# Performance work log

Measured on AMD Instinct MI355X. Metric: run time of the kernel, lower is better.

The kernel has to match this reference:

```python
import jax, jax.numpy as jnp
import numpy as np

N_VOX = 100000
C_IN = 32
C_OUT = 64
GRID = 96  # voxel grid extent per axis
K = 27     # 3x3x3 kernel offsets
BN_EPS = 1e-5


def _build_neighbor_idx(rng):
    """Sample N_VOX unique active voxels in a GRID^3 volume and build the
    rulebook: for each voxel, the row index of each of its 27 neighbors
    (kernel offsets in {-1,0,1}^3), or -1 if that neighbor is inactive."""
    total = GRID ** 3
    flat = rng.choice(total, size=N_VOX, replace=False).astype(np.int64)
    z = flat // (GRID * GRID)
    y = (flat // GRID) % GRID
    x = flat % GRID
    # dense lookup table: flat coord -> row index (or -1)
    lut = np.full(total, -1, dtype=np.int32)
    lut[flat] = np.arange(N_VOX, dtype=np.int32)
    offs = np.array([(dz, dy, dx)
                     for dz in (-1, 0, 1)
                     for dy in (-1, 0, 1)
                     for dx in (-1, 0, 1)], dtype=np.int64)  # [27,3]
    nz = z[:, None] + offs[None, :, 0]
    ny = y[:, None] + offs[None, :, 1]
    nx = x[:, None] + offs[None, :, 2]
    inb = ((nz >= 0) & (nz < GRID) & (ny >= 0) & (ny < GRID)
           & (nx >= 0) & (nx < GRID))
    nflat = np.where(inb, nz * GRID * GRID + ny * GRID + nx, 0)
    nidx = lut[nflat]                       # [N,27]
    nidx = np.where(inb, nidx, -1).astype(np.int32)
    return nidx


def setup_inputs() -> dict:
    key = jax.random.key(0)
    k_f, k_w = jax.random.split(key)
    rng = np.random.default_rng(0)
    neighbor_idx = jnp.asarray(_build_neighbor_idx(rng))  # [N,27] int32
    features = jax.random.normal(k_f, (N_VOX, C_IN), dtype=jnp.float32)
    # per-kernel-offset conv weights, kaiming-ish scale
    W = jax.random.normal(k_w, (K, C_IN, C_OUT), dtype=jnp.float32)
    W = W * (2.0 / (K * C_IN)) ** 0.5
    gamma = jnp.ones((C_OUT,), dtype=jnp.float32)
    beta = jnp.zeros((C_OUT,), dtype=jnp.float32)
    return {"features": features, "neighbor_idx": neighbor_idx,
            "W": W, "gamma": gamma, "beta": beta}


def reference(features, neighbor_idx, W, gamma, beta):
    # --- sparse (submanifold) 3D conv: gather -> GEMM ---
    mask = neighbor_idx >= 0                               # [N,27]
    safe_idx = jnp.where(mask, neighbor_idx, 0)
    gathered = features[safe_idx]                          # [N,27,Cin]
    gathered = gathered * mask[..., None].astype(features.dtype)
    out = jnp.einsum('nkc,kcd->nd', gathered, W)           # [N,Cout]
    # --- batch norm over active voxels (training-mode stats) ---
    mean = jnp.mean(out, axis=0)
    var = jnp.var(out, axis=0)
    out = (out - mean) * jax.lax.rsqrt(var + BN_EPS) * gamma + beta
    # --- ReLU ---
    return jax.nn.relu(out)
```

## Files before the change

### kernel.cpp

```cpp
#include <hip/hip_runtime.h>
#include <hip/hip_bf16.h>

#define N_VOX 100000
#define C_IN  32
#define C_OUT 64
#define KOFF  27
#define CONV_T 512
#define GRID_C 256
#define VPB    256
#define NT     391
#define NB_FB  782
#define WT_BLOCKS 216
#define WT_HALFS (KOFF * C_OUT * C_IN)
#define WT_BYTES (WT_HALFS * 2)

typedef __attribute__((ext_vector_type(8))) short bf16x8_t;
typedef __attribute__((ext_vector_type(4))) float f32x4_t;

__device__ __forceinline__ short f2bf(float f) {
    __hip_bfloat16 h = __float2bfloat16(f);
    return __builtin_bit_cast(short, h);
}
__device__ __forceinline__ float bf2f(unsigned short u) {
    return __builtin_bit_cast(float, (unsigned)u << 16);
}

__global__ void prep_kernel(const float* __restrict__ W,
                            unsigned short* __restrict__ Wt,
                            const float* __restrict__ feat,
                            unsigned short* __restrict__ fb) {
    int bid = blockIdx.x;
    if (bid < WT_BLOCKS) {
        int i = bid * 256 + threadIdx.x;
        int c = i & 31;
        int d = (i >> 5) & 63;
        int k = i >> 11;
        int dst = i ^ ((d & 7) << 3);
        Wt[dst] = (unsigned short)f2bf(W[k * (C_IN * C_OUT) + c * C_OUT + d]);
    } else {
        int t = (bid - WT_BLOCKS) * 256 + threadIdx.x;
        const int total8 = ((N_VOX + 1) * C_IN) / 8;
        if (t >= total8) return;
        int e = t * 8;
        bf16x8_t o;
        if (e < N_VOX * C_IN) {
            const f32x4_t* fp = (const f32x4_t*)(feat + e);
            f32x4_t f0 = fp[0], f1 = fp[1];
            o[0] = f2bf(f0[0]); o[1] = f2bf(f0[1]); o[2] = f2bf(f0[2]); o[3] = f2bf(f0[3]);
            o[4] = f2bf(f1[0]); o[5] = f2bf(f1[1]); o[6] = f2bf(f1[2]); o[7] = f2bf(f1[3]);
        } else {
            o = (bf16x8_t)(short)0;
        }
        *(bf16x8_t*)(fb + e) = o;
    }
}

#define GLOAD(dst, voff)                                                      \
    asm volatile("global_load_dwordx4 %0, %1, %2"                             \
                 : "=v"(dst) : "v"(voff), "s"(feat_bf))

#define VMW(n) do {                                                           \
    asm volatile("s_waitcnt vmcnt(" #n ")" ::: "memory");                     \
    __builtin_amdgcn_sched_barrier(0);                                        \
} while (0)

template <bool OUTBF>
__global__ __launch_bounds__(CONV_T, 2) void conv_kernel(
    const unsigned short* __restrict__ feat_bf,
    const int* __restrict__ nidx,
    const unsigned short* __restrict__ WtG,
    float* __restrict__ outf, unsigned short* __restrict__ outb,
    float* __restrict__ partials)
{
    __shared__ unsigned short wt_lds[WT_HALFS];
    __shared__ float lsum[8][C_OUT];
    __shared__ float lsq[8][C_OUT];

    const int tid  = threadIdx.x;
    const int wid  = tid >> 6;
    const int lane = tid & 63;
    const int colr = lane & 15;
    const int kch  = lane >> 4;

    for (int j = tid; j < WT_HALFS / 8; j += CONV_T)
        ((bf16x8_t*)wt_lds)[j] = ((const bf16x8_t*)WtG)[j];
    __syncthreads();

    float psum[4] = {0.f, 0.f, 0.f, 0.f};
    float psq[4]  = {0.f, 0.f, 0.f, 0.f};

    const int b  = blockIdx.x;
    const int bs = ((b & 7) << 5) | (b >> 3);
    const int rr0 = NT % GRID_C;
    const int t0  = bs + (bs < rr0 ? bs : rr0);
    const int cnt = 1 + (bs < rr0 ? 1 : 0);

    for (int ti = 0; ti < cnt; ++ti) {
        const int base = (t0 + ti) * VPB + wid * 32;

        unsigned off[54];
        #pragma unroll
        for (int m = 0; m < 2; ++m) {
            int vx = base + m * 16 + colr;
            bool val = vx < N_VOX;
            const int* nr = nidx + (val ? vx : 0) * KOFF;
            int force = val ? 0 : -1;
            #pragma unroll
            for (int k = 0; k < KOFF; ++k) {
                int id = nr[k] | force;
                int s = (id < 0) ? N_VOX : id;
                off[k * 2 + m] = ((unsigned)s << 6) + (unsigned)(kch << 4);
            }
        }
        __builtin_amdgcn_sched_barrier(0);

        f32x4_t acc0[4], acc1[4];
        #pragma unroll
        for (int t = 0; t < 4; ++t) { acc0[t] = (f32x4_t)0.0f; acc1[t] = (f32x4_t)0.0f; }

        bf16x8_t a[12];
        #pragma unroll
        for (int u = 0; u < 12; ++u) GLOAD(a[u], off[u]);
        __builtin_amdgcn_sched_barrier(0);

        #pragma unroll
        for (int c = 0; c < 9; ++c) {
            if (c < 8) { VMW(6); } else { VMW(0); }
            const int ab = (c & 1) * 6;
            #pragma unroll
            for (int j = 0; j < 3; ++j) {
                const int kk = c * 3 + j;
                #pragma unroll
                for (int t = 0; t < 4; ++t) {
                    const int rw = t * 16 + colr;
                    int o = (kk << 12) + (rw << 6) + (kch << 4);
                    o ^= (rw & 7) << 4;
                    bf16x8_t bb = *(const bf16x8_t*)((const char*)wt_lds + o);
                    acc0[t] = __builtin_amdgcn_mfma_f32_16x16x32_bf16(
                        a[ab + j * 2 + 0], bb, acc0[t], 0, 0, 0);
                    acc1[t] = __builtin_amdgcn_mfma_f32_16x16x32_bf16(
                        a[ab + j * 2 + 1], bb, acc1[t], 0, 0, 0);
                }
            }
            if (c + 2 < 9) {
                const int nb2 = ((c + 2) & 1) * 6;
                #pragma unroll
                for (int u = 0; u < 6; ++u) GLOAD(a[nb2 + u], off[(c + 2) * 6 + u]);
                __builtin_amdgcn_sched_barrier(0);
            }
        }

        #pragma unroll
        for (int t = 0; t < 4; ++t) {
            #pragma unroll
            for (int i = 0; i < 4; ++i) {
                int v0 = base + kch * 4 + i;
                int v1 = v0 + 16;
                int ch = t * 16 + colr;
                float x0 = acc0[t][i], x1 = acc1[t][i];
                if (v0 < N_VOX) {
                    if constexpr (OUTBF) outb[v0 * C_OUT + ch] = (unsigned short)f2bf(x0);
                    else                 outf[v0 * C_OUT + ch] = x0;
                }
                if (v1 < N_VOX) {
                    if constexpr (OUTBF) outb[v1 * C_OUT + ch] = (unsigned short)f2bf(x1);
                    else                 outf[v1 * C_OUT + ch] = x1;
                }
                psum[t] += x0 + x1;
                psq[t]  += x0 * x0 + x1 * x1;
            }
        }
    }

    #pragma unroll
    for (int t = 0; t < 4; ++t) {
        psum[t] += __shfl_xor(psum[t], 16);
        psum[t] += __shfl_xor(psum[t], 32);
        psq[t]  += __shfl_xor(psq[t], 16);
        psq[t]  += __shfl_xor(psq[t], 32);
    }
    if (lane < 16) {
        #pragma unroll
        for (int t = 0; t < 4; ++t) {
            lsum[wid][t * 16 + lane] = psum[t];
            lsq[wid][t * 16 + lane]  = psq[t];
        }
    }
    __syncthreads();
    if (tid < 128) {
        int c = tid & 63;
        float s = 0.f;
        if (tid < 64) {
            #pragma unroll
            for (int w = 0; w < 8; ++w) s += lsum[w][c];
        } else {
            #pragma unroll
            for (int w = 0; w < 8; ++w) s += lsq[w][c];
        }
        partials[tid * GRID_C + b] = s;
    }
}

__global__ __launch_bounds__(CONV_T) void conv_fb_kernel(
    const float* __restrict__ feat,
    const int* __restrict__ nidx,
    const unsigned short* __restrict__ WtG,
    float* __restrict__ outf, float* __restrict__ partials)
{
    __shared__ unsigned short wt_lds[WT_HALFS];
    __shared__ float lsum[8][C_OUT];
    __shared__ float lsq[8][C_OUT];

    const int tid  = threadIdx.x;
    const int wid  = tid >> 6;
    const int lane = tid & 63;
    const int colr = lane & 15;
    const int kch  = lane >> 4;
    const int base = blockIdx.x * 128 + wid * 16;
    const int vox  = base + colr;
    const bool valid = (vox < N_VOX);
    const int* nrow = nidx + (valid ? vox : 0) * KOFF;

    for (int j = tid; j < WT_HALFS / 8; j += CONV_T)
        ((bf16x8_t*)wt_lds)[j] = ((const bf16x8_t*)WtG)[j];
    __syncthreads();

    f32x4_t acc[4];
    #pragma unroll
    for (int t = 0; t < 4; ++t) acc[t] = (f32x4_t)0.0f;

    for (int k = 0; k < KOFF; ++k) {
        int idx = valid ? nrow[k] : -1;
        bf16x8_t av = (bf16x8_t)(short)0;
        if (idx >= 0) {
            const f32x4_t* fp = (const f32x4_t*)(feat + (idx << 5) + kch * 8);
            f32x4_t f0 = fp[0], f1 = fp[1];
            av[0] = f2bf(f0[0]); av[1] = f2bf(f0[1]);
            av[2] = f2bf(f0[2]); av[3] = f2bf(f0[3]);
            av[4] = f2bf(f1[0]); av[5] = f2bf(f1[1]);
            av[6] = f2bf(f1[2]); av[7] = f2bf(f1[3]);
        }
        #pragma unroll
        for (int t = 0; t < 4; ++t) {
            int rw = t * 16 + colr;
            int o = (k << 12) + (rw << 6) + (kch << 4);
            o ^= (rw & 7) << 4;
            bf16x8_t bb = *(const bf16x8_t*)((const char*)wt_lds + o);
            acc[t] = __builtin_amdgcn_mfma_f32_16x16x32_bf16(av, bb, acc[t], 0, 0, 0);
        }
    }

    float psum[4], psq[4];
    #pragma unroll
    for (int t = 0; t < 4; ++t) { psum[t] = 0.f; psq[t] = 0.f; }
    #pragma unroll
    for (int t = 0; t < 4; ++t) {
        #pragma unroll
        for (int i = 0; i < 4; ++i) {
            int v = base + kch * 4 + i;
            float x = acc[t][i];
            if (v < N_VOX) outf[v * C_OUT + t * 16 + colr] = x;
            psum[t] += x;
            psq[t]  += x * x;
        }
    }
    #pragma unroll
    for (int t = 0; t < 4; ++t) {
        psum[t] += __shfl_xor(psum[t], 16);
        psum[t] += __shfl_xor(psum[t], 32);
        psq[t]  += __shfl_xor(psq[t], 16);
        psq[t]  += __shfl_xor(psq[t], 32);
    }
    if (lane < 16) {
        #pragma unroll
        for (int t = 0; t < 4; ++t) {
            lsum[wid][t * 16 + lane] = psum[t];
            lsq[wid][t * 16 + lane]  = psq[t];
        }
    }
    __syncthreads();
    if (tid < 128) {
        int c = tid & 63;
        float s = 0.f;
        if (tid < 64) {
            #pragma unroll
            for (int w = 0; w < 8; ++w) s += lsum[w][c];
        } else {
            #pragma unroll
            for (int w = 0; w < 8; ++w) s += lsq[w][c];
        }
        partials[tid * NB_FB + blockIdx.x] = s;
    }
}

__global__ __launch_bounds__(256) void stats_kernel(
    const float* __restrict__ partials, int nb,
    const float* __restrict__ gamma, const float* __restrict__ beta,
    float* __restrict__ ss)
{
    __shared__ float bs[4], bq[4];
    const int c = blockIdx.x;
    const float* ps = partials + c * nb;
    const float* pq = partials + (64 + c) * nb;
    float s = 0.f, q = 0.f;
    for (int i = threadIdx.x; i < nb; i += 256) {
        s += ps[i];
        q += pq[i];
    }
    #pragma unroll
    for (int o = 1; o < 64; o <<= 1) {
        s += __shfl_xor(s, o);
        q += __shfl_xor(q, o);
    }
    int wid = threadIdx.x >> 6, lane = threadIdx.x & 63;
    if (lane == 0) { bs[wid] = s; bq[wid] = q; }
    __syncthreads();
    if (threadIdx.x == 0) {
        float S = bs[0] + bs[1] + bs[2] + bs[3];
        float Q = bq[0] + bq[1] + bq[2] + bq[3];
        float mean = S * (1.0f / N_VOX);
        float var  = Q * (1.0f / N_VOX) - mean * mean;
        float inv  = rsqrtf(var + 1e-5f);
        float sc   = gamma[c] * inv;
        ss[c]      = sc;
        ss[64 + c] = beta[c] - mean * sc;
    }
}

__global__ void bn_relu_b_kernel(const unsigned short* __restrict__ cbf,
                                 const float* __restrict__ ss,
                                 float* __restrict__ out) {
    int i = blockIdx.x * 256 + threadIdx.x;
    bf16x8_t v = ((const bf16x8_t*)cbf)[i];
    int d0 = (i * 8) & 63;
    f32x4_t sc0 = *(const f32x4_t*)(ss + d0);
    f32x4_t sc1 = *(const f32x4_t*)(ss + d0 + 4);
    f32x4_t sh0 = *(const f32x4_t*)(ss + 64 + d0);
    f32x4_t sh1 = *(const f32x4_t*)(ss + 64 + d0 + 4);
    f32x4_t o0, o1;
    #pragma unroll
    for (int j = 0; j < 4; ++j) {
        o0[j] = fmaxf(bf2f((unsigned short)v[j]) * sc0[j] + sh0[j], 0.f);
        o1[j] = fmaxf(bf2f((unsigned short)v[j + 4]) * sc1[j] + sh1[j], 0.f);
    }
    ((f32x4_t*)out)[2 * i]     = o0;
    ((f32x4_t*)out)[2 * i + 1] = o1;
}

__global__ void bn_relu_f_kernel(float* __restrict__ out,
                                 const float* __restrict__ ss) {
    int i = blockIdx.x * 256 + threadIdx.x;
    f32x4_t v = ((f32x4_t*)out)[i];
    int d0 = (i * 4) & 63;
    f32x4_t sc = *(const f32x4_t*)(ss + d0);
    f32x4_t sh = *(const f32x4_t*)(ss + 64 + d0);
    #pragma unroll
    for (int j = 0; j < 4; ++j) v[j] = fmaxf(v[j] * sc[j] + sh[j], 0.f);
    ((f32x4_t*)out)[i] = v;
}

extern "C" void kernel_launch(void* const* d_in, const int* in_sizes, int n_in,
                              void* d_out, int out_size, void* d_ws, size_t ws_size,
                              hipStream_t stream) {
    const float* feat  = (const float*)d_in[0];
    const int*   nidx  = (const int*)d_in[1];
    const float* W     = (const float*)d_in[2];
    const float* gamma = (const float*)d_in[3];
    const float* beta  = (const float*)d_in[4];
    float* out = (float*)d_out;

    char* ws = (char*)d_ws;
    const size_t wt_bytes  = WT_BYTES;
    const size_t fb_bytes  = (size_t)(N_VOX + 1) * C_IN * 2;
    const size_t cb_bytes  = (size_t)N_VOX * C_OUT * 2;
    const size_t pt_bytes  = (size_t)128 * NB_FB * 4;

    const bool bf_ok  = ws_size >= wt_bytes + fb_bytes + pt_bytes + 512;
    const bool cb_ok  = ws_size >= wt_bytes + fb_bytes + cb_bytes + pt_bytes + 512;

    unsigned short* Wt = (unsigned short*)ws;
    unsigned short* feat_bf = (unsigned short*)(ws + wt_bytes);
    unsigned short* cbf = (unsigned short*)(ws + wt_bytes + fb_bytes);
    float* partials;
    if (cb_ok)       partials = (float*)(ws + wt_bytes + fb_bytes + cb_bytes);
    else if (bf_ok)  partials = (float*)(ws + wt_bytes + fb_bytes);
    else             partials = (float*)(ws + wt_bytes);
    float* ss = partials + 128 * NB_FB;

    if (bf_ok) {
        int feat_blocks = (((N_VOX + 1) * C_IN) / 8 + 255) / 256;
        prep_kernel<<<WT_BLOCKS + feat_blocks, 256, 0, stream>>>(W, Wt, feat, feat_bf);
        if (cb_ok)
            conv_kernel<true><<<GRID_C, CONV_T, 0, stream>>>(
                feat_bf, nidx, Wt, out, cbf, partials);
        else
            conv_kernel<false><<<GRID_C, CONV_T, 0, stream>>>(
                feat_bf, nidx, Wt, out, cbf, partials);
        stats_kernel<<<C_OUT, 256, 0, stream>>>(partials, GRID_C, gamma, beta, ss);
    } else {
        prep_kernel<<<WT_BLOCKS, 256, 0, stream>>>(W, Wt, feat, Wt);
        conv_fb_kernel<<<NB_FB, CONV_T, 0, stream>>>(feat, nidx, Wt, out, partials);
        stats_kernel<<<C_OUT, 256, 0, stream>>>(partials, NB_FB, gamma, beta, ss);
    }
    if (cb_ok)
        bn_relu_b_kernel<<<N_VOX * C_OUT / 8 / 256, 256, 0, stream>>>(cbf, ss, out);
    else
        bn_relu_f_kernel<<<N_VOX * C_OUT / 4 / 256, 256, 0, stream>>>(out, ss);
}
```

Measured before the change: 42.48 us.

## Fuse conv, BN statistics and BN+ReLU via grid-wide atomic barrier

```diff
diff --git a/kernel.cpp b/kernel.cpp
--- a/kernel.cpp
+++ b/kernel.cpp
@@ -20,9 +20,6 @@
 __device__ __forceinline__ short f2bf(float f) {
     __hip_bfloat16 h = __float2bfloat16(f);
     return __builtin_bit_cast(short, h);
-}
-__device__ __forceinline__ float bf2f(unsigned short u) {
-    return __builtin_bit_cast(float, (unsigned)u << 16);
 }
 
 __global__ void prep_kernel(const float* __restrict__ W,
@@ -64,13 +61,84 @@
     __builtin_amdgcn_sched_barrier(0);                                        \
 } while (0)
 
-template <bool OUTBF>
-__global__ __launch_bounds__(CONV_T, 2) void conv_kernel(
+__device__ __forceinline__ void process_tile(
+    int tileIdx, const unsigned short* __restrict__ feat_bf,
+    const int* __restrict__ nidx, const unsigned short* wt_lds,
+    int wid, int colr, int kch,
+    f32x4_t (&acc0)[4], f32x4_t (&acc1)[4],
+    float (&psum)[4], float (&psq)[4])
+{
+    const int base = tileIdx * VPB + wid * 32;
+
+    unsigned off[54];
+    #pragma unroll
+    for (int m = 0; m < 2; ++m) {
+        int vx = base + m * 16 + colr;
+        bool val = vx < N_VOX;
+        const int* nr = nidx + (val ? vx : 0) * KOFF;
+        int force = val ? 0 : -1;
+        #pragma unroll
+        for (int k = 0; k < KOFF; ++k) {
+            int id = nr[k] | force;
+            int s = (id < 0) ? N_VOX : id;
+            off[k * 2 + m] = ((unsigned)s << 6) + (unsigned)(kch << 4);
+        }
+    }
+    __builtin_amdgcn_sched_barrier(0);
+
+    #pragma unroll
+    for (int t = 0; t < 4; ++t) { acc0[t] = (f32x4_t)0.0f; acc1[t] = (f32x4_t)0.0f; }
+
+    bf16x8_t a[12];
+    #pragma unroll
+    for (int u = 0; u < 12; ++u) GLOAD(a[u], off[u]);
+    __builtin_amdgcn_sched_barrier(0);
+
+    #pragma unroll
+    for (int c = 0; c < 9; ++c) {
+        if (c < 8) { VMW(6); } else { VMW(0); }
+        const int ab = (c & 1) * 6;
+        #pragma unroll
+        for (int j = 0; j < 3; ++j) {
+            const int kk = c * 3 + j;
+            #pragma unroll
+            for (int t = 0; t < 4; ++t) {
+                const int rw = t * 16 + colr;
+                int o = (kk << 12) + (rw << 6) + (kch << 4);
+                o ^= (rw & 7) << 4;
+                bf16x8_t bb = *(const bf16x8_t*)((const char*)wt_lds + o);
+                acc0[t] = __builtin_amdgcn_mfma_f32_16x16x32_bf16(
+                    a[ab + j * 2 + 0], bb, acc0[t], 0, 0, 0);
+                acc1[t] = __builtin_amdgcn_mfma_f32_16x16x32_bf16(
+                    a[ab + j * 2 + 1], bb, acc1[t], 0, 0, 0);
+            }
+        }
+        if (c + 2 < 9) {
+            const int nb2 = ((c + 2) & 1) * 6;
+            #pragma unroll
+            for (int u = 0; u < 6; ++u) GLOAD(a[nb2 + u], off[(c + 2) * 6 + u]);
+            __builtin_amdgcn_sched_barrier(0);
+        }
+    }
+
+    #pragma unroll
+    for (int t = 0; t < 4; ++t) {
+        #pragma unroll
+        for (int i = 0; i < 4; ++i) {
+            float x0 = acc0[t][i], x1 = acc1[t][i];
+            psum[t] += x0 + x1;
+            psq[t]  += x0 * x0 + x1 * x1;
+        }
+    }
+}
+
+__global__ __launch_bounds__(CONV_T, 2) void conv_fused_kernel(
     const unsigned short* __restrict__ feat_bf,
     const int* __restrict__ nidx,
     const unsigned short* __restrict__ WtG,
-    float* __restrict__ outf, unsigned short* __restrict__ outb,
-    float* __restrict__ partials)
+    const float* __restrict__ gamma, const float* __restrict__ beta,
+    float* __restrict__ out, float* __restrict__ partials,
+    unsigned int* counter)
 {
     __shared__ unsigned short wt_lds[WT_HALFS];
     __shared__ float lsum[8][C_OUT];
@@ -93,84 +161,12 @@
     const int bs = ((b & 7) << 5) | (b >> 3);
     const int rr0 = NT % GRID_C;
     const int t0  = bs + (bs < rr0 ? bs : rr0);
-    const int cnt = 1 + (bs < rr0 ? 1 : 0);
-
-    for (int ti = 0; ti < cnt; ++ti) {
-        const int base = (t0 + ti) * VPB + wid * 32;
-
-        unsigned off[54];
-        #pragma unroll
-        for (int m = 0; m < 2; ++m) {
-            int vx = base + m * 16 + colr;
-            bool val = vx < N_VOX;
-            const int* nr = nidx + (val ? vx : 0) * KOFF;
-            int force = val ? 0 : -1;
-            #pragma unroll
-            for (int k = 0; k < KOFF; ++k) {
-                int id = nr[k] | force;
-                int s = (id < 0) ? N_VOX : id;
-                off[k * 2 + m] = ((unsigned)s << 6) + (unsigned)(kch << 4);
-            }
-        }
-        __builtin_amdgcn_sched_barrier(0);
-
-        f32x4_t acc0[4], acc1[4];
-        #pragma unroll
-        for (int t = 0; t < 4; ++t) { acc0[t] = (f32x4_t)0.0f; acc1[t] = (f32x4_t)0.0f; }
-
-        bf16x8_t a[12];
-        #pragma unroll
-        for (int u = 0; u < 12; ++u) GLOAD(a[u], off[u]);
-        __builtin_amdgcn_sched_barrier(0);
-
-        #pragma unroll
-        for (int c = 0; c < 9; ++c) {
-            if (c < 8) { VMW(6); } else { VMW(0); }
-            const int ab = (c & 1) * 6;
-            #pragma unroll
-            for (int j = 0; j < 3; ++j) {
-                const int kk = c * 3 + j;
-                #pragma unroll
-                for (int t = 0; t < 4; ++t) {
-                    const int rw = t * 16 + colr;
-                    int o = (kk << 12) + (rw << 6) + (kch << 4);
-                    o ^= (rw & 7) << 4;
-                    bf16x8_t bb = *(const bf16x8_t*)((const char*)wt_lds + o);
-                    acc0[t] = __builtin_amdgcn_mfma_f32_16x16x32_bf16(
-                        a[ab + j * 2 + 0], bb, acc0[t], 0, 0, 0);
-                    acc1[t] = __builtin_amdgcn_mfma_f32_16x16x32_bf16(
-                        a[ab + j * 2 + 1], bb, acc1[t], 0, 0, 0);
-                }
-            }
-            if (c + 2 < 9) {
-                const int nb2 = ((c + 2) & 1) * 6;
-                #pragma unroll
-                for (int u = 0; u < 6; ++u) GLOAD(a[nb2 + u], off[(c + 2) * 6 + u]);
-                __builtin_amdgcn_sched_barrier(0);
-            }
-        }
-
-        #pragma unroll
-        for (int t = 0; t < 4; ++t) {
-            #pragma unroll
-            for (int i = 0; i < 4; ++i) {
-                int v0 = base + kch * 4 + i;
-                int v1 = v0 + 16;
-                int ch = t * 16 + colr;
-                float x0 = acc0[t][i], x1 = acc1[t][i];
-                if (v0 < N_VOX) {
-                    if constexpr (OUTBF) outb[v0 * C_OUT + ch] = (unsigned short)f2bf(x0);
-                    else                 outf[v0 * C_OUT + ch] = x0;
-                }
-                if (v1 < N_VOX) {
-                    if constexpr (OUTBF) outb[v1 * C_OUT + ch] = (unsigned short)f2bf(x1);
-                    else                 outf[v1 * C_OUT + ch] = x1;
-                }
-                psum[t] += x0 + x1;
-                psq[t]  += x0 * x0 + x1 * x1;
-            }
-        }
-    }
+    const bool two = (bs < rr0);
+
+    f32x4_t a0A[4], a1A[4], a0B[4], a1B[4];
+    process_tile(t0, feat_bf, nidx, wt_lds, wid, colr, kch, a0A, a1A, psum, psq);
+    if (two)
+        process_tile(t0 + 1, feat_bf, nidx, wt_lds, wid, colr, kch, a0B, a1B, psum, psq);
 
     #pragma unroll
     for (int t = 0; t < 4; ++t) {
@@ -198,6 +194,73 @@
             for (int w = 0; w < 8; ++w) s += lsq[w][c];
         }
         partials[tid * GRID_C + b] = s;
+    }
+
+    __threadfence();
+    __syncthreads();
+    if (tid == 0) {
+        __hip_atomic_fetch_add(counter, 1u, __ATOMIC_ACQ_REL, __HIP_MEMORY_SCOPE_AGENT);
+        while (__hip_atomic_load(counter, __ATOMIC_ACQUIRE, __HIP_MEMORY_SCOPE_AGENT) < GRID_C)
+            __builtin_amdgcn_s_sleep(2);
+    }
+    __syncthreads();
+    __threadfence();
+
+    float* red = &lsum[0][0];
+    float* stg = &lsq[0][0];
+    {
+        int row = tid & 127;
+        int grp = tid >> 7;
+        const float* pr = partials + row * GRID_C + grp * 64;
+        float s = 0.f;
+        #pragma unroll 8
+        for (int j2 = 0; j2 < 64; ++j2) s += pr[j2];
+        red[grp * 128 + row] = s;
+    }
+    __syncthreads();
+    if (tid < 128)
+        stg[tid] = red[tid] + red[128 + tid] + red[256 + tid] + red[384 + tid];
+    __syncthreads();
+    if (tid < 64) {
+        float S = stg[tid], Q = stg[64 + tid];
+        float mean = S * (1.0f / N_VOX);
+        float var  = Q * (1.0f / N_VOX) - mean * mean;
+        float inv  = rsqrtf(var + 1e-5f);
+        float sc   = gamma[tid] * inv;
+        stg[128 + tid] = sc;
+        stg[192 + tid] = beta[tid] - mean * sc;
+    }
+    __syncthreads();
+
+    const int baseA = t0 * VPB + wid * 32;
+    #pragma unroll
+    for (int t = 0; t < 4; ++t) {
+        int ch = t * 16 + colr;
+        float sc = stg[128 + ch];
+        float sh = stg[192 + ch];
+        #pragma unroll
+        for (int i = 0; i < 4; ++i) {
+            int v0 = baseA + kch * 4 + i;
+            int v1 = v0 + 16;
+            if (v0 < N_VOX) out[v0 * C_OUT + ch] = fmaxf(a0A[t][i] * sc + sh, 0.f);
+            if (v1 < N_VOX) out[v1 * C_OUT + ch] = fmaxf(a1A[t][i] * sc + sh, 0.f);
+        }
+    }
+    if (two) {
+        const int baseB = baseA + VPB;
+        #pragma unroll
+        for (int t = 0; t < 4; ++t) {
+            int ch = t * 16 + colr;
+            float sc = stg[128 + ch];
+            float sh = stg[192 + ch];
+            #pragma unroll
+            for (int i = 0; i < 4; ++i) {
+                int v0 = baseB + kch * 4 + i;
+                int v1 = v0 + 16;
+                if (v0 < N_VOX) out[v0 * C_OUT + ch] = fmaxf(a0B[t][i] * sc + sh, 0.f);
+                if (v1 < N_VOX) out[v1 * C_OUT + ch] = fmaxf(a1B[t][i] * sc + sh, 0.f);
+            }
+        }
     }
 }
 
@@ -327,26 +390,6 @@
     }
 }
 
-__global__ void bn_relu_b_kernel(const unsigned short* __restrict__ cbf,
-                                 const float* __restrict__ ss,
-                                 float* __restrict__ out) {
-    int i = blockIdx.x * 256 + threadIdx.x;
-    bf16x8_t v = ((const bf16x8_t*)cbf)[i];
-    int d0 = (i * 8) & 63;
-    f32x4_t sc0 = *(const f32x4_t*)(ss + d0);
-    f32x4_t sc1 = *(const f32x4_t*)(ss + d0 + 4);
-    f32x4_t sh0 = *(const f32x4_t*)(ss + 64 + d0);
-    f32x4_t sh1 = *(const f32x4_t*)(ss + 64 + d0 + 4);
-    f32x4_t o0, o1;
-    #pragma unroll
-    for (int j = 0; j < 4; ++j) {
-        o0[j] = fmaxf(bf2f((unsigned short)v[j]) * sc0[j] + sh0[j], 0.f);
-        o1[j] = fmaxf(bf2f((unsigned short)v[j + 4]) * sc1[j] + sh1[j], 0.f);
-    }
-    ((f32x4_t*)out)[2 * i]     = o0;
-    ((f32x4_t*)out)[2 * i + 1] = o1;
-}
-
 __global__ void bn_relu_f_kernel(float* __restrict__ out,
                                  const float* __restrict__ ss) {
     int i = blockIdx.x * 256 + threadIdx.x;
@@ -372,38 +415,26 @@
     char* ws = (char*)d_ws;
     const size_t wt_bytes  = WT_BYTES;
     const size_t fb_bytes  = (size_t)(N_VOX + 1) * C_IN * 2;
-    const size_t cb_bytes  = (size_t)N_VOX * C_OUT * 2;
     const size_t pt_bytes  = (size_t)128 * NB_FB * 4;
 
-    const bool bf_ok  = ws_size >= wt_bytes + fb_bytes + pt_bytes + 512;
-    const bool cb_ok  = ws_size >= wt_bytes + fb_bytes + cb_bytes + pt_bytes + 512;
+    const bool bf_ok = ws_size >= wt_bytes + fb_bytes + pt_bytes + 1024;
 
     unsigned short* Wt = (unsigned short*)ws;
     unsigned short* feat_bf = (unsigned short*)(ws + wt_bytes);
-    unsigned short* cbf = (unsigned short*)(ws + wt_bytes + fb_bytes);
-    float* partials;
-    if (cb_ok)       partials = (float*)(ws + wt_bytes + fb_bytes + cb_bytes);
-    else if (bf_ok)  partials = (float*)(ws + wt_bytes + fb_bytes);
-    else             partials = (float*)(ws + wt_bytes);
+    float* partials = (float*)(ws + wt_bytes + fb_bytes);
     float* ss = partials + 128 * NB_FB;
+    unsigned int* counter = (unsigned int*)(ws + wt_bytes + fb_bytes + pt_bytes + 512);
 
     if (bf_ok) {
+        hipMemsetAsync((void*)counter, 0, 4, stream);
         int feat_blocks = (((N_VOX + 1) * C_IN) / 8 + 255) / 256;
         prep_kernel<<<WT_BLOCKS + feat_blocks, 256, 0, stream>>>(W, Wt, feat, feat_bf);
-        if (cb_ok)
-            conv_kernel<true><<<GRID_C, CONV_T, 0, stream>>>(
-                feat_bf, nidx, Wt, out, cbf, partials);
-        else
-            conv_kernel<false><<<GRID_C, CONV_T, 0, stream>>>(
-                feat_bf, nidx, Wt, out, cbf, partials);
-        stats_kernel<<<C_OUT, 256, 0, stream>>>(partials, GRID_C, gamma, beta, ss);
+        conv_fused_kernel<<<GRID_C, CONV_T, 0, stream>>>(
+            feat_bf, nidx, Wt, gamma, beta, out, partials, counter);
     } else {
         prep_kernel<<<WT_BLOCKS, 256, 0, stream>>>(W, Wt, feat, Wt);
         conv_fb_kernel<<<NB_FB, CONV_T, 0, stream>>>(feat, nidx, Wt, out, partials);
         stats_kernel<<<C_OUT, 256, 0, stream>>>(partials, NB_FB, gamma, beta, ss);
-    }
-    if (cb_ok)
-        bn_relu_b_kernel<<<N_VOX * C_OUT / 8 / 256, 256, 0, stream>>>(cbf, ss, out);
-    else
         bn_relu_f_kernel<<<N_VOX * C_OUT / 4 / 256, 256, 0, stream>>>(out, ss);
-}
+    }
+}
```

Result: slower. 160.3 us (+277.5%).
